# Performance work log

Measured on AMD Instinct MI355X. Metric: run time of the kernel, lower is better.

## Reference

```python
import jax, jax.numpy as jnp
import numpy as np

NVIEW = 6
N = 6400        # nodes (hardcoded in source: torch.empty(6400, 6))
D = 2048        # input_dim
H = 512         # hidden_dim
C = 256         # common_dim
E = 204800      # edges per view (avg degree 32)


def spmm(h, src, dst, val):
    # sparse_adj @ h : gather source rows, scale by edge value, scatter-add to dst
    msg = val[:, None] * h[src]              # [E, F]
    return jax.ops.segment_sum(msg, dst, num_segments=N)


def setup_inputs() -> dict:
    key = jax.random.key(0)
    ks = jax.random.split(key, 12)
    x = jax.random.normal(ks[0], (NVIEW, N, D), dtype=jnp.float32)
    adj_src = jax.random.randint(ks[1], (NVIEW, E), 0, N, dtype=jnp.int32)
    adj_dst = jax.random.randint(ks[2], (NVIEW, E), 0, N, dtype=jnp.int32)
    # normalized-adjacency-like positive values, scaled ~1/degree to keep activations sane
    adj_val = jax.random.uniform(ks[3], (NVIEW, E), dtype=jnp.float32) / 32.0
    # glorot-ish scaling
    Wb = jax.random.normal(ks[4], (NVIEW, D, H), dtype=jnp.float32) / np.sqrt(D)
    Wo = jax.random.normal(ks[5], (NVIEW, H, H), dtype=jnp.float32) / np.sqrt(H)
    Wf = jax.random.normal(ks[6], (NVIEW, H, H), dtype=jnp.float32) / np.sqrt(H)
    Wc0 = jax.random.normal(ks[7], (D, C), dtype=jnp.float32) / np.sqrt(D)
    Wc1 = jax.random.normal(ks[8], (C, C), dtype=jnp.float32) / np.sqrt(C)
    Wc2 = jax.random.normal(ks[9], (C, C), dtype=jnp.float32) / np.sqrt(C)
    gate_w = jax.random.normal(ks[10], (NVIEW, NVIEW, H + C), dtype=jnp.float32) / np.sqrt(H + C)
    gate_b = jax.random.normal(ks[11], (NVIEW, NVIEW), dtype=jnp.float32) * 0.01
    return {"x": x, "adj_val": adj_val, "Wb": Wb, "Wo": Wo, "Wf": Wf,
            "Wc0": Wc0, "Wc1": Wc1, "Wc2": Wc2, "gate_w": gate_w, "gate_b": gate_b,
            "adj_src": adj_src, "adj_dst": adj_dst}


def reference(x, adj_val, Wb, Wo, Wf, Wc0, Wc1, Wc2, gate_w, gate_b, adj_src, adj_dst):
    zs = []
    for v in range(NVIEW):
        src, dst, val = adj_src[v], adj_dst[v], adj_val[v]
        # view-specific 3-layer GCN (relu, relu, identity)
        hidden = jax.nn.relu(spmm(x[v] @ Wb[v], src, dst, val))   # [N, H]
        mid    = jax.nn.relu(spmm(hidden @ Wo[v], src, dst, val)) # [N, H]
        final  = spmm(mid @ Wf[v], src, dst, val)                 # [N, H]
        z_v = (hidden + mid + final) / 3.0                        # layer_agg == 'mean'
        # shared common 3-layer GCN
        c = jax.nn.relu(spmm(x[v] @ Wc0, src, dst, val))          # [N, C]
        c = jax.nn.relu(spmm(c @ Wc1, src, dst, val))
        c = jax.nn.relu(spmm(c @ Wc2, src, dst, val))
        zs.append(jnp.concatenate([c, z_v], axis=1))              # [N, C+H]
    Z = jnp.stack(zs, axis=0)                                     # [V, N, C+H]
    # gate scores: score_k[:, i] = Linear_{k,i}(z_i)
    scores = jnp.einsum('inf,kif->kni', Z, gate_w) + gate_b[:, None, :]  # [V, N, V]
    scores = jax.nn.softmax(scores, axis=-1)
    z_global = jnp.einsum('kni,inf->knf', scores, Z)              # [V, N, C+H]
    return (z_global, Z)
```

## Files before the change

kernel.cpp:

```cpp
#include <hip/hip_runtime.h>
#include <hip/hip_bf16.h>

#define NVIEW 6
#define NN    6400
#define DD    2048
#define HH    512
#define CC    256
#define EE    204800
#define ZF    768

typedef __bf16 bf16x8 __attribute__((ext_vector_type(8)));
typedef __bf16 bf16x4 __attribute__((ext_vector_type(4)));
typedef float  f32x4  __attribute__((ext_vector_type(4)));

__device__ __forceinline__ float b2f(unsigned short u) {
  union { unsigned int i; float f; } c; c.i = ((unsigned int)u) << 16; return c.f;
}

__device__ __forceinline__ void glds16(const void* g, void* l) {
  __builtin_amdgcn_global_load_lds((const __attribute__((address_space(1))) void*)g,
                                   (__attribute__((address_space(3))) void*)l, 16, 0, 0);
}

__global__ void k_hist(const int* __restrict__ dst, int* __restrict__ hist) {
  int e = blockIdx.x * 256 + threadIdx.x;
  int v = blockIdx.y;
  if (e < EE) atomicAdd(&hist[v * NN + dst[(size_t)v * EE + e]], 1);
}

__global__ __launch_bounds__(1024) void k_scan(const int* __restrict__ hist,
                                               int* __restrict__ rp) {
  int v = blockIdx.x;
  const int* h = hist + v * NN;
  int* r = rp + v * (NN + 1);
  __shared__ int part[1024];
  int t = threadIdx.x;
  const int CH = 7;
  int base = t * CH;
  int loc[CH];
  int s = 0;
#pragma unroll
  for (int i = 0; i < CH; i++) {
    int idx = base + i;
    int val = (idx < NN) ? h[idx] : 0;
    loc[i] = s;
    s += val;
  }
  part[t] = s;
  __syncthreads();
  for (int off = 1; off < 1024; off <<= 1) {
    int x = (t >= off) ? part[t - off] : 0;
    __syncthreads();
    part[t] += x;
    __syncthreads();
  }
  int pre = (t == 0) ? 0 : part[t - 1];
#pragma unroll
  for (int i = 0; i < CH; i++) {
    int idx = base + i;
    if (idx < NN) r[idx] = pre + loc[i];
  }
  if (t == 1023) r[NN] = part[1023];
}

__global__ void k_cursor(const int* __restrict__ rp, int* __restrict__ cur) {
  int i = blockIdx.x * 256 + threadIdx.x;
  if (i < NVIEW * NN) {
    int v = i / NN, n = i - v * NN;
    cur[i] = rp[v * (NN + 1) + n];
  }
}

__global__ void k_scatter(const int* __restrict__ src, const int* __restrict__ dstA,
                          const float* __restrict__ val, int* __restrict__ cur,
                          int2* __restrict__ sedge) {
  int e = blockIdx.x * 256 + threadIdx.x;
  int v = blockIdx.y;
  if (e < EE) {
    size_t idx = (size_t)v * EE + e;
    int d = dstA[idx];
    int pos = atomicAdd(&cur[v * NN + d], 1);
    sedge[(size_t)v * EE + pos] = make_int2(src[idx], __float_as_int(val[idx]));
  }
}

__global__ __launch_bounds__(256) void k_cvt(const float* __restrict__ in,
                                             __bf16* __restrict__ out) {
  size_t i = (size_t)blockIdx.x * 256 + threadIdx.x;
  float4 q = ((const float4*)in)[i];
  bf16x4 o;
  o[0] = (__bf16)q.x; o[1] = (__bf16)q.y; o[2] = (__bf16)q.z; o[3] = (__bf16)q.w;
  *(bf16x4*)(out + i * 4) = o;
}

__global__ __launch_bounds__(256) void k_tw(const float* __restrict__ in,
                                            __bf16* __restrict__ out, int K, int N,
                                            size_t inSB, size_t outSB) {
  __shared__ float sh[32][33];
  int b = blockIdx.z;
  int k0 = blockIdx.x * 32, n0 = blockIdx.y * 32;
  int tx = threadIdx.x & 31, ty = threadIdx.x >> 5;
  const float* I = in + (size_t)b * inSB;
  __bf16* O = out + (size_t)b * outSB;
#pragma unroll
  for (int r = 0; r < 4; r++)
    sh[ty + r * 8][tx] = I[(size_t)(k0 + ty + r * 8) * N + n0 + tx];
  __syncthreads();
#pragma unroll
  for (int r = 0; r < 4; r++)
    O[(size_t)(n0 + ty + r * 8) * K + k0 + tx] = (__bf16)sh[tx][ty + r * 8];
}

__global__ __launch_bounds__(512, 2) void k_g256(
    const __bf16* __restrict__ A, const __bf16* __restrict__ BT,
    __bf16* __restrict__ C, int K, int Nc, int nbn, int bpv, int wPerView)
{
  __shared__ __bf16 ldsv[65536];
  int tid = threadIdx.x, lane = tid & 63, w = tid >> 6;

  int nwg = gridDim.x;
  int q8 = nwg >> 3, r8 = nwg & 7;
  int orig = blockIdx.x;
  int xcd = orig & 7, j = orig >> 3;
  int swz = (xcd < r8 ? xcd * (q8 + 1) : r8 * (q8 + 1) + (xcd - r8) * q8) + j;
  int v = swz / bpv; int rr = swz - v * bpv;
  int bm = rr / nbn; int bn = rr - bm * nbn;

  const __bf16* Av = A + (size_t)v * NN * K + (size_t)(bm * 256) * K;
  const __bf16* Bv = BT + (wPerView ? (size_t)v * Nc * K : 0) + (size_t)(bn * 256) * K;

  f32x4 acc[8][4];
#pragma unroll
  for (int m = 0; m < 8; m++)
#pragma unroll
    for (int n = 0; n < 4; n++) acc[m][n] = (f32x4){0.f, 0.f, 0.f, 0.f};

  const int wr = (w >> 2) * 128, wc = (w & 3) * 64;
  const int gq = lane >> 4, l15 = lane & 15;

  bf16x8 aFr[2][4], bFr[2][4];

#define STAGE_UNIT(Gp, LOFF, KH, KT)                                          \
  {                                                                           \
    _Pragma("unroll")                                                         \
    for (int g2 = 0; g2 < 2; g2++) {                                          \
      int chunk = (KH) * 1024 + (w + g2 * 8) * 64 + lane;                     \
      int row_ = chunk & 255, kkg_ = chunk >> 8;                              \
      glds16(Gp + (size_t)row_ * K + (KT) * 64 + kkg_ * 8,                    \
             ldsv + (LOFF) + chunk * 8);                                      \
    }                                                                         \
  }

#define RD_A(SET, BUFO, KK, MH)                                               \
  {                                                                           \
    _Pragma("unroll")                                                         \
    for (int m = 0; m < 4; m++)                                               \
      aFr[SET][m] = *(const bf16x8*)&ldsv[(BUFO) +                            \
          (((KK) * 4 + gq) * 256 + wr + (MH) * 64 + m * 16 + l15) * 8];       \
  }

#define RD_B(SET, BUFO, KK)                                                   \
  {                                                                           \
    _Pragma("unroll")                                                         \
    for (int n = 0; n < 4; n++)                                               \
      bFr[SET][n] = *(const bf16x8*)&ldsv[(BUFO) + 16384 +                    \
          (((KK) * 4 + gq) * 256 + wc + n * 16 + l15) * 8];                   \
  }

#define MFMA_HALF(ASET, BSET, MH, M0)                                         \
  {                                                                           \
    __builtin_amdgcn_s_setprio(1);                                            \
    _Pragma("unroll")                                                         \
    for (int m = (M0); m < (M0) + 2; m++)                                     \
      _Pragma("unroll")                                                       \
      for (int n = 0; n < 4; n++)                                             \
        acc[(MH) * 4 + m][n] = __builtin_amdgcn_mfma_f32_16x16x32_bf16(       \
            aFr[ASET][m], bFr[BSET][n], acc[(MH) * 4 + m][n], 0, 0, 0);       \
    __builtin_amdgcn_s_setprio(0);                                            \
  }

#define PH_TOP()                                                              \
  {                                                                           \
    __builtin_amdgcn_s_barrier();                                             \
    asm volatile("s_waitcnt lgkmcnt(0)" ::: "memory");                        \
    __builtin_amdgcn_sched_barrier(0);                                        \
  }

  const int nt = K >> 6;
  const int ni = nt >> 1;

  STAGE_UNIT(Av, 0,     0, 0);
  STAGE_UNIT(Bv, 16384, 0, 0);
  STAGE_UNIT(Av, 0,     1, 0);
  STAGE_UNIT(Bv, 16384, 1, 0);
  STAGE_UNIT(Av, 32768, 0, 1);
  STAGE_UNIT(Bv, 49152, 0, 1);
  asm volatile("s_waitcnt vmcnt(4)" ::: "memory");
  __builtin_amdgcn_s_barrier();
  RD_A(1, 0, 0, 0); RD_B(0, 0, 0);

  for (int i = 0; i < ni; ++i) {
    int t1 = 2 * i + 1, t2 = 2 * i + 2, t3 = 2 * i + 3;
    bool more = (i + 1 < ni);
    PH_TOP();
    MFMA_HALF(1, 0, 0, 0);
    RD_A(0, 0, 0, 1);
    STAGE_UNIT(Av, 32768, 1, t1);
    asm volatile("s_waitcnt vmcnt(6)" ::: "memory");
    MFMA_HALF(1, 0, 0, 2);
    PH_TOP();
    MFMA_HALF(0, 0, 1, 0);
    RD_A(1, 0, 1, 0); RD_B(1, 0, 1);
    STAGE_UNIT(Bv, 49152, 1, t1);
    MFMA_HALF(0, 0, 1, 2);
    PH_TOP();
    MFMA_HALF(1, 1, 0, 0);
    RD_A(0, 0, 1, 1);
    if (more) {
      STAGE_UNIT(Av, 0, 0, t2);
      asm volatile("s_waitcnt vmcnt(6)" ::: "memory");
    } else {
      asm volatile("s_waitcnt vmcnt(4)" ::: "memory");
    }
    MFMA_HALF(1, 1, 0, 2);
    PH_TOP();
    MFMA_HALF(0, 1, 1, 0);
    RD_A(1, 32768, 0, 0); RD_B(0, 32768, 0);
    if (more) STAGE_UNIT(Bv, 16384, 0, t2);
    MFMA_HALF(0, 1, 1, 2);
    PH_TOP();
    MFMA_HALF(1, 0, 0, 0);
    RD_A(0, 32768, 0, 1);
    if (more) {
      STAGE_UNIT(Av, 0, 1, t2);
      asm volatile("s_waitcnt vmcnt(6)" ::: "memory");
    } else {
      asm volatile("s_waitcnt vmcnt(0)" ::: "memory");
    }
    MFMA_HALF(1, 0, 0, 2);
    PH_TOP();
    MFMA_HALF(0, 0, 1, 0);
    RD_A(1, 32768, 1, 0); RD_B(1, 32768, 1);
    if (more) STAGE_UNIT(Bv, 16384, 1, t2);
    MFMA_HALF(0, 0, 1, 2);
    PH_TOP();
    MFMA_HALF(1, 1, 0, 0);
    RD_A(0, 32768, 1, 1);
    if (more) {
      STAGE_UNIT(Av, 32768, 0, t3);
      asm volatile("s_waitcnt vmcnt(6)" ::: "memory");
    }
    MFMA_HALF(1, 1, 0, 2);
    PH_TOP();
    MFMA_HALF(0, 1, 1, 0);
    if (more) {
      RD_A(1, 0, 0, 0); RD_B(0, 0, 0);
      STAGE_UNIT(Bv, 49152, 0, t3);
    }
    MFMA_HALF(0, 1, 1, 2);
  }

#undef STAGE_UNIT
#undef RD_A
#undef RD_B
#undef MFMA_HALF
#undef PH_TOP

  __bf16* Cv = C + (size_t)v * NN * Nc;
#pragma unroll
  for (int m = 0; m < 8; m++) {
    int rbase = bm * 256 + wr + m * 16 + (lane >> 4) * 4;
#pragma unroll
    for (int q = 0; q < 4; q++) {
      __bf16* cp = Cv + (size_t)(rbase + q) * Nc + bn * 256 + wc + l15;
#pragma unroll
      for (int n = 0; n < 4; n++) cp[n * 16] = (__bf16)acc[m][n][q];
    }
  }
}

template <int LDIN, int FOFF, int F, int CHUNKS, int MODE>
__global__ __launch_bounds__(256) void k_spmm(
    const __bf16* __restrict__ in, const int* __restrict__ rp,
    const int2* __restrict__ sedge, void* __restrict__ out,
    const __bf16* __restrict__ h1, const __bf16* __restrict__ h2)
{
  int id = blockIdx.x;
  int s = id & 7, j = id >> 3;
  int ch, v, rowblk;
  if (CHUNKS == 2) {
    ch = s >> 2; int q = s & 3;
    v = j / 400; int t = j - v * 400;
    rowblk = t * 4 + q;
  } else {
    ch = 0;
    v = j / 200; int t = j - v * 200;
    rowblk = t * 8 + s;
  }
  int wid = threadIdx.x >> 6, lane = threadIdx.x & 63;
  int n = rowblk * 4 + wid;
  int f0 = ch * 256 + lane * 4;

  const int* rpv = rp + v * (NN + 1);
  int e = rpv[n], end = rpv[n + 1];
  const int2* ev = sedge + (size_t)v * EE;
  const __bf16* inv = in + (size_t)v * NN * LDIN + FOFF;

  float a0 = 0.f, a1 = 0.f, a2 = 0.f, a3 = 0.f;
  for (; e + 8 <= end; e += 8) {
    int2 ee[8]; ushort4 rrv[8];
#pragma unroll
    for (int u = 0; u < 8; u++) ee[u] = ev[e + u];
#pragma unroll
    for (int u = 0; u < 8; u++)
      rrv[u] = *(const ushort4*)(inv + (size_t)ee[u].x * LDIN + f0);
#pragma unroll
    for (int u = 0; u < 8; u++) {
      float wv = __int_as_float(ee[u].y);
      a0 += wv * b2f(rrv[u].x); a1 += wv * b2f(rrv[u].y);
      a2 += wv * b2f(rrv[u].z); a3 += wv * b2f(rrv[u].w);
    }
  }
  if (e + 4 <= end) {
    int2 ee[4]; ushort4 rrv[4];
#pragma unroll
    for (int u = 0; u < 4; u++) ee[u] = ev[e + u];
#pragma unroll
    for (int u = 0; u < 4; u++)
      rrv[u] = *(const ushort4*)(inv + (size_t)ee[u].x * LDIN + f0);
#pragma unroll
    for (int u = 0; u < 4; u++) {
      float wv = __int_as_float(ee[u].y);
      a0 += wv * b2f(rrv[u].x); a1 += wv * b2f(rrv[u].y);
      a2 += wv * b2f(rrv[u].z); a3 += wv * b2f(rrv[u].w);
    }
    e += 4;
  }
  for (; e < end; ++e) {
    int2 e0 = ev[e];
    float w0 = __int_as_float(e0.y);
    ushort4 r0 = *(const ushort4*)(inv + (size_t)e0.x * LDIN + f0);
    a0 += w0 * b2f(r0.x); a1 += w0 * b2f(r0.y);
    a2 += w0 * b2f(r0.z); a3 += w0 * b2f(r0.w);
  }

  if (MODE == 0) {
    __bf16* o = (__bf16*)out + ((size_t)v * NN + n) * F + f0;
    bf16x4 ov;
    ov[0] = (__bf16)fmaxf(a0, 0.f); ov[1] = (__bf16)fmaxf(a1, 0.f);
    ov[2] = (__bf16)fmaxf(a2, 0.f); ov[3] = (__bf16)fmaxf(a3, 0.f);
    *(bf16x4*)o = ov;
  } else if (MODE == 1) {
    float* o = (float*)out + ((size_t)v * NN + n) * ZF + f0;
    o[0] = fmaxf(a0, 0.f); o[1] = fmaxf(a1, 0.f);
    o[2] = fmaxf(a2, 0.f); o[3] = fmaxf(a3, 0.f);
  } else {
    const __bf16* hh = h1 + ((size_t)v * NN + n) * 512 + f0;
    const __bf16* mm = h2 + ((size_t)v * NN + n) * 512 + f0;
    ushort4 hu = *(const ushort4*)hh;
    ushort4 mu = *(const ushort4*)mm;
    float* o = (float*)out + ((size_t)v * NN + n) * ZF + CC + f0;
    o[0] = (b2f(hu.x) + b2f(mu.x) + a0) * (1.f / 3.f);
    o[1] = (b2f(hu.y) + b2f(mu.y) + a1) * (1.f / 3.f);
    o[2] = (b2f(hu.z) + b2f(mu.z) + a2) * (1.f / 3.f);
    o[3] = (b2f(hu.w) + b2f(mu.w) + a3) * (1.f / 3.f);
  }
}

__global__ __launch_bounds__(256) void k_gate(
    const float* __restrict__ Z, const float* __restrict__ gw,
    const float* __restrict__ gb, float* __restrict__ zg)
{
  __shared__ float Zl[NVIEW * ZF];
  __shared__ float sred[36];
  __shared__ float pl[36];
  int n = blockIdx.x, tid = threadIdx.x;

  for (int idx = tid; idx < NVIEW * ZF; idx += 256) {
    int i = idx / ZF, f = idx - i * ZF;
    Zl[idx] = Z[((size_t)i * NN + n) * ZF + f];
  }
  if (tid < 36) sred[tid] = 0.f;
  __syncthreads();

  float acc[36];
#pragma unroll
  for (int p = 0; p < 36; p++) acc[p] = 0.f;
#pragma unroll
  for (int q = 0; q < 3; q++) {
    int f = tid + q * 256;
    float zv[NVIEW];
#pragma unroll
    for (int i = 0; i < NVIEW; i++) zv[i] = Zl[i * ZF + f];
#pragma unroll
    for (int k = 0; k < NVIEW; k++)
#pragma unroll
      for (int i = 0; i < NVIEW; i++)
        acc[k * 6 + i] += zv[i] * gw[(k * 6 + i) * ZF + f];
  }
  int lane = tid & 63;
#pragma unroll
  for (int p = 0; p < 36; p++) {
    float x = acc[p];
    x += __shfl_down(x, 32, 64);
    x += __shfl_down(x, 16, 64);
    x += __shfl_down(x, 8, 64);
    x += __shfl_down(x, 4, 64);
    x += __shfl_down(x, 2, 64);
    x += __shfl_down(x, 1, 64);
    if (lane == 0) atomicAdd(&sred[p], x);
  }
  __syncthreads();

  if (tid < NVIEW) {
    int k = tid;
    float sc[NVIEW];
    float mx = -1e30f;
#pragma unroll
    for (int i = 0; i < NVIEW; i++) {
      sc[i] = sred[k * 6 + i] + gb[k * 6 + i];
      mx = fmaxf(mx, sc[i]);
    }
    float sum = 0.f;
#pragma unroll
    for (int i = 0; i < NVIEW; i++) { sc[i] = __expf(sc[i] - mx); sum += sc[i]; }
    float inv = 1.f / sum;
#pragma unroll
    for (int i = 0; i < NVIEW; i++) pl[k * 6 + i] = sc[i] * inv;
  }
  __syncthreads();

#pragma unroll
  for (int q = 0; q < 3; q++) {
    int f = tid + q * 256;
    float zv[NVIEW];
#pragma unroll
    for (int i = 0; i < NVIEW; i++) zv[i] = Zl[i * ZF + f];
#pragma unroll
    for (int k = 0; k < NVIEW; k++) {
      float o = 0.f;
#pragma unroll
      for (int i = 0; i < NVIEW; i++) o += pl[k * 6 + i] * zv[i];
      zg[((size_t)k * NN + n) * ZF + f] = o;
    }
  }
}

extern "C" void kernel_launch(void* const* d_in, const int* in_sizes, int n_in,
                              void* d_out, int out_size, void* d_ws, size_t ws_size,
                              hipStream_t stream) {
  const float* x    = (const float*)d_in[0];
  const float* aval = (const float*)d_in[1];
  const float* Wb   = (const float*)d_in[2];
  const float* Wo   = (const float*)d_in[3];
  const float* Wf   = (const float*)d_in[4];
  const float* Wc0  = (const float*)d_in[5];
  const float* Wc1  = (const float*)d_in[6];
  const float* Wc2  = (const float*)d_in[7];
  const float* gw   = (const float*)d_in[8];
  const float* gb   = (const float*)d_in[9];
  const int*   asrc = (const int*)d_in[10];
  const int*   adst = (const int*)d_in[11];

  float* zg = (float*)d_out;
  float* Z  = zg + (size_t)NVIEW * NN * ZF;
  __bf16* xb = (__bf16*)d_out;

  char* w = (char*)d_ws;
  auto alloc = [&](size_t bytes) {
    char* p = w;
    w += (bytes + 255) & ~(size_t)255;
    return p;
  };
  int*    hist  = (int*)alloc((size_t)NVIEW * NN * 4);
  int*    rp    = (int*)alloc((size_t)NVIEW * (NN + 1) * 4);
  int2*   sedge = (int2*)alloc((size_t)NVIEW * EE * 8);
  __bf16* Wfu   = (__bf16*)alloc((size_t)NVIEW * ZF * DD * 2);
  __bf16* WoT   = (__bf16*)alloc((size_t)NVIEW * HH * HH * 2);
  __bf16* WfT   = (__bf16*)alloc((size_t)NVIEW * HH * HH * 2);
  __bf16* Wc1T  = (__bf16*)alloc((size_t)CC * CC * 2);
  __bf16* Wc2T  = (__bf16*)alloc((size_t)CC * CC * 2);
  __bf16* tf768 = (__bf16*)alloc((size_t)NVIEW * NN * ZF * 2);
  __bf16* t512b = (__bf16*)alloc((size_t)NVIEW * NN * HH * 2);
  __bf16* hidb  = (__bf16*)alloc((size_t)NVIEW * NN * HH * 2);
  __bf16* midb  = (__bf16*)alloc((size_t)NVIEW * NN * HH * 2);
  __bf16* tcb   = (__bf16*)alloc((size_t)NVIEW * NN * CC * 2);
  __bf16* cbb   = (__bf16*)alloc((size_t)NVIEW * NN * CC * 2);

  (void)hipMemsetAsync(hist, 0, (size_t)NVIEW * NN * 4, stream);
  k_hist<<<dim3(800, NVIEW), 256, 0, stream>>>(adst, hist);
  k_scan<<<NVIEW, 1024, 0, stream>>>(hist, rp);
  k_cursor<<<150, 256, 0, stream>>>(rp, hist);
  k_scatter<<<dim3(800, NVIEW), 256, 0, stream>>>(asrc, adst, aval, hist, sedge);

  k_cvt<<<76800, 256, 0, stream>>>(x, xb);
  k_tw<<<dim3(64, 16, NVIEW), 256, 0, stream>>>(Wb, Wfu, DD, HH,
                                                (size_t)DD * HH, (size_t)ZF * DD);
  k_tw<<<dim3(64, 8, NVIEW), 256, 0, stream>>>(Wc0, Wfu + (size_t)HH * DD, DD, CC,
                                               0, (size_t)ZF * DD);
  k_tw<<<dim3(16, 16, NVIEW), 256, 0, stream>>>(Wo, WoT, HH, HH,
                                                (size_t)HH * HH, (size_t)HH * HH);
  k_tw<<<dim3(16, 16, NVIEW), 256, 0, stream>>>(Wf, WfT, HH, HH,
                                                (size_t)HH * HH, (size_t)HH * HH);
  k_tw<<<dim3(8, 8, 1), 256, 0, stream>>>(Wc1, Wc1T, CC, CC, 0, 0);
  k_tw<<<dim3(8, 8, 1), 256, 0, stream>>>(Wc2, Wc2T, CC, CC, 0, 0);

  k_g256<<<450, 512, 0, stream>>>(xb, Wfu, tf768, DD, ZF, 3, 75, 1);
  k_spmm<768, 0, 512, 2, 0><<<19200, 256, 0, stream>>>(tf768, rp, sedge, hidb, nullptr, nullptr);
  k_spmm<768, 512, 256, 1, 0><<<9600, 256, 0, stream>>>(tf768, rp, sedge, cbb, nullptr, nullptr);

  k_g256<<<300, 512, 0, stream>>>(hidb, WoT, t512b, HH, HH, 2, 50, 1);
  k_spmm<512, 0, 512, 2, 0><<<19200, 256, 0, stream>>>(t512b, rp, sedge, midb, nullptr, nullptr);
  k_g256<<<150, 512, 0, stream>>>(cbb, Wc1T, tcb, CC, CC, 1, 25, 0);
  k_spmm<256, 0, 256, 1, 0><<<9600, 256, 0, stream>>>(tcb, rp, sedge, cbb, nullptr, nullptr);
  k_g256<<<300, 512, 0, stream>>>(midb, WfT, t512b, HH, HH, 2, 50, 1);
  k_spmm<512, 0, 512, 2, 2><<<19200, 256, 0, stream>>>(t512b, rp, sedge, Z, hidb, midb);
  k_g256<<<150, 512, 0, stream>>>(cbb, Wc2T, tcb, CC, CC, 1, 25, 0);
  k_spmm<256, 0, 256, 1, 1><<<9600, 256, 0, stream>>>(tcb, rp, sedge, Z, nullptr, nullptr);

  k_gate<<<NN, 256, 0, stream>>>(Z, gw, gb, zg);
}
```

Baseline: 1.356 ms.

## Restructure GEMM LDS layout and replace interleaved read/MFMA ping-pong with phased schedule

```diff
diff --git a/kernel.cpp b/kernel.cpp
--- a/kernel.cpp
+++ b/kernel.cpp
@@ -138,52 +138,50 @@
   const int wr = (w >> 2) * 128, wc = (w & 3) * 64;
   const int gq = lane >> 4, l15 = lane & 15;
 
-  bf16x8 aFr[2][4], bFr[2][4];
-
 #define STAGE_UNIT(Gp, LOFF, KH, KT)                                          \
   {                                                                           \
     _Pragma("unroll")                                                         \
     for (int g2 = 0; g2 < 2; g2++) {                                          \
-      int chunk = (KH) * 1024 + (w + g2 * 8) * 64 + lane;                     \
-      int row_ = chunk & 255, kkg_ = chunk >> 8;                              \
-      glds16(Gp + (size_t)row_ * K + (KT) * 64 + kkg_ * 8,                    \
-             ldsv + (LOFF) + chunk * 8);                                      \
+      int u = g2 * 512 + tid;                                                 \
+      int row_ = ((u >> 5) << 3) | (u & 7);                                   \
+      int kkgl_ = (u >> 3) & 3;                                               \
+      glds16(Gp + (size_t)row_ * K + (KT) * 64 + (KH) * 32 + kkgl_ * 8,       \
+             ldsv + (LOFF) + (KH) * 8192 + u * 8);                            \
     }                                                                         \
   }
 
-#define RD_A(SET, BUFO, KK, MH)                                               \
+#define PH_READS(KK, MH, LOADB)                                               \
   {                                                                           \
     _Pragma("unroll")                                                         \
-    for (int m = 0; m < 4; m++)                                               \
-      aFr[SET][m] = *(const bf16x8*)&ldsv[(BUFO) +                            \
-          (((KK) * 4 + gq) * 256 + wr + (MH) * 64 + m * 16 + l15) * 8];       \
-  }
-
-#define RD_B(SET, BUFO, KK)                                                   \
-  {                                                                           \
-    _Pragma("unroll")                                                         \
-    for (int n = 0; n < 4; n++)                                               \
-      bFr[SET][n] = *(const bf16x8*)&ldsv[(BUFO) + 16384 +                    \
-          (((KK) * 4 + gq) * 256 + wc + n * 16 + l15) * 8];                   \
-  }
-
-#define MFMA_HALF(ASET, BSET, MH, M0)                                         \
-  {                                                                           \
-    __builtin_amdgcn_s_setprio(1);                                            \
-    _Pragma("unroll")                                                         \
-    for (int m = (M0); m < (M0) + 2; m++)                                     \
+    for (int m = 0; m < 4; m++) {                                             \
+      int ra = wr + (MH) * 64 + m * 16 + l15;                                 \
+      aF[m] = *(const bf16x8*)&Ab[(KK) * 8192 + (ra >> 3) * 256 + gq * 64 +   \
+                                  (ra & 7) * 8];                              \
+    }                                                                         \
+    if (LOADB) {                                                              \
       _Pragma("unroll")                                                       \
-      for (int n = 0; n < 4; n++)                                             \
-        acc[(MH) * 4 + m][n] = __builtin_amdgcn_mfma_f32_16x16x32_bf16(       \
-            aFr[ASET][m], bFr[BSET][n], acc[(MH) * 4 + m][n], 0, 0, 0);       \
-    __builtin_amdgcn_s_setprio(0);                                            \
-  }
-
-#define PH_TOP()                                                              \
+      for (int n = 0; n < 4; n++) {                                           \
+        int rb = wc + n * 16 + l15;                                           \
+        bF[n] = *(const bf16x8*)&Bb[(KK) * 8192 + (rb >> 3) * 256 + gq * 64 + \
+                                    (rb & 7) * 8];                            \
+      }                                                                       \
+    }                                                                         \
+  }
+
+#define PH_MFMA(MH)                                                           \
   {                                                                           \
     __builtin_amdgcn_s_barrier();                                             \
     asm volatile("s_waitcnt lgkmcnt(0)" ::: "memory");                        \
     __builtin_amdgcn_sched_barrier(0);                                        \
+    __builtin_amdgcn_s_setprio(1);                                            \
+    _Pragma("unroll")                                                         \
+    for (int m = 0; m < 4; m++)                                               \
+      _Pragma("unroll")                                                       \
+      for (int n = 0; n < 4; n++)                                             \
+        acc[(MH) * 4 + m][n] = __builtin_amdgcn_mfma_f32_16x16x32_bf16(       \
+            aF[m], bF[n], acc[(MH) * 4 + m][n], 0, 0, 0);                     \
+    __builtin_amdgcn_s_setprio(0);                                            \
+    __builtin_amdgcn_s_barrier();                                             \
   }
 
   const int nt = K >> 6;
@@ -197,74 +195,51 @@
   STAGE_UNIT(Bv, 49152, 0, 1);
   asm volatile("s_waitcnt vmcnt(4)" ::: "memory");
   __builtin_amdgcn_s_barrier();
-  RD_A(1, 0, 0, 0); RD_B(0, 0, 0);
-
+
+  bf16x8 aF[4], bF[4];
   for (int i = 0; i < ni; ++i) {
     int t1 = 2 * i + 1, t2 = 2 * i + 2, t3 = 2 * i + 3;
     bool more = (i + 1 < ni);
-    PH_TOP();
-    MFMA_HALF(1, 0, 0, 0);
-    RD_A(0, 0, 0, 1);
+    const __bf16* Ab = ldsv;
+    const __bf16* Bb = ldsv + 16384;
+    PH_READS(0, 0, true);
     STAGE_UNIT(Av, 32768, 1, t1);
     asm volatile("s_waitcnt vmcnt(6)" ::: "memory");
-    MFMA_HALF(1, 0, 0, 2);
-    PH_TOP();
-    MFMA_HALF(0, 0, 1, 0);
-    RD_A(1, 0, 1, 0); RD_B(1, 0, 1);
-    STAGE_UNIT(Bv, 49152, 1, t1);
-    MFMA_HALF(0, 0, 1, 2);
-    PH_TOP();
-    MFMA_HALF(1, 1, 0, 0);
-    RD_A(0, 0, 1, 1);
+    PH_MFMA(0);
+    PH_READS(0, 1, false); STAGE_UNIT(Bv, 49152, 1, t1);              PH_MFMA(1);
+    PH_READS(1, 0, true);
     if (more) {
       STAGE_UNIT(Av, 0, 0, t2);
       asm volatile("s_waitcnt vmcnt(6)" ::: "memory");
     } else {
       asm volatile("s_waitcnt vmcnt(4)" ::: "memory");
     }
-    MFMA_HALF(1, 1, 0, 2);
-    PH_TOP();
-    MFMA_HALF(0, 1, 1, 0);
-    RD_A(1, 32768, 0, 0); RD_B(0, 32768, 0);
-    if (more) STAGE_UNIT(Bv, 16384, 0, t2);
-    MFMA_HALF(0, 1, 1, 2);
-    PH_TOP();
-    MFMA_HALF(1, 0, 0, 0);
-    RD_A(0, 32768, 0, 1);
+    PH_MFMA(0);
+    PH_READS(1, 1, false); if (more) STAGE_UNIT(Bv, 16384, 0, t2);    PH_MFMA(1);
+    Ab = ldsv + 32768; Bb = ldsv + 49152;
+    PH_READS(0, 0, true);
     if (more) {
       STAGE_UNIT(Av, 0, 1, t2);
       asm volatile("s_waitcnt vmcnt(6)" ::: "memory");
     } else {
       asm volatile("s_waitcnt vmcnt(0)" ::: "memory");
     }
-    MFMA_HALF(1, 0, 0, 2);
-    PH_TOP();
-    MFMA_HALF(0, 0, 1, 0);
-    RD_A(1, 32768, 1, 0); RD_B(1, 32768, 1);
-    if (more) STAGE_UNIT(Bv, 16384, 1, t2);
-    MFMA_HALF(0, 0, 1, 2);
-    PH_TOP();
-    MFMA_HALF(1, 1, 0, 0);
-    RD_A(0, 32768, 1, 1);
+    PH_MFMA(0);
+    PH_READS(0, 1, false); if (more) STAGE_UNIT(Bv, 16384, 1, t2);    PH_MFMA(1);
+    PH_READS(1, 0, true);
     if (more) {
       STAGE_UNIT(Av, 32768, 0, t3);
       asm volatile("s_waitcnt vmcnt(6)" ::: "memory");
     }
-    MFMA_HALF(1, 1, 0, 2);
-    PH_TOP();
-    MFMA_HALF(0, 1, 1, 0);
-    if (more) {
-      RD_A(1, 0, 0, 0); RD_B(0, 0, 0);
-      STAGE_UNIT(Bv, 49152, 0, t3);
-    }
-    MFMA_HALF(0, 1, 1, 2);
+    PH_MFMA(0);
+    PH_READS(1, 1, false);
+    if (more) STAGE_UNIT(Bv, 49152, 0, t3);
+    PH_MFMA(1);
   }
 
 #undef STAGE_UNIT
-#undef RD_A
-#undef RD_B
-#undef MFMA_HALF
-#undef PH_TOP
+#undef PH_READS
+#undef PH_MFMA
 
   __bf16* Cv = C + (size_t)v * NN * Nc;
 #pragma unroll
```

Measured after the change: 1.165 ms. 14.1% less time.
